# Kernel tuning notes

Hardware: AMD Instinct MI355X
Metric: run time of the kernel (lower is better)

## Reference

```python
import jax, jax.numpy as jnp
import numpy as np

D_MODEL = 1024
HEADS = 16
HEAD_DIM = D_MODEL // HEADS
D_FF = 4096
ADA_DIM = 16
GAMMA_SCALE = 1.0
LN_EPS = 1e-5
ROPE_BASE = 10000.0


def setup_inputs() -> dict:
    key = jax.random.key(0)
    ks = jax.random.split(key, 20)
    s = 0.02
    B, S = 4, 1024
    inp = {
        "src_reps": jax.random.normal(ks[0], (B, S, D_MODEL), jnp.float32),
        "src_mask": jnp.ones((B, S), dtype=bool),
        "compact_style": jax.random.normal(ks[1], (B, ADA_DIM), jnp.float32),
        # adaLN modulation params (stored as [in, out]; torch Linear uses [out, in])
        "ada0_w": jax.random.normal(ks[2], (ADA_DIM, 3 * D_MODEL), jnp.float32) * s,
        "ada0_b": jax.random.normal(ks[3], (3 * D_MODEL,), jnp.float32) * s,
        "ada1_w": jax.random.normal(ks[4], (ADA_DIM, 3 * D_MODEL), jnp.float32) * s,
        "ada1_b": jax.random.normal(ks[5], (3 * D_MODEL,), jnp.float32) * s,
        # attention params
        "wq": jax.random.normal(ks[6], (D_MODEL, D_MODEL), jnp.float32) * s,
        "bq": jnp.zeros((D_MODEL,), jnp.float32),
        "wk": jax.random.normal(ks[7], (D_MODEL, D_MODEL), jnp.float32) * s,
        "bk": jnp.zeros((D_MODEL,), jnp.float32),
        "wv": jax.random.normal(ks[8], (D_MODEL, D_MODEL), jnp.float32) * s,
        "bv": jnp.zeros((D_MODEL,), jnp.float32),
        "wo": jax.random.normal(ks[9], (D_MODEL, D_MODEL), jnp.float32) * s,
        "bo": jnp.zeros((D_MODEL,), jnp.float32),
        # FFN params
        "w1": jax.random.normal(ks[10], (D_MODEL, D_FF), jnp.float32) * s,
        "b1": jnp.zeros((D_FF,), jnp.float32),
        "w2": jax.random.normal(ks[11], (D_FF, D_MODEL), jnp.float32) * s,
        "b2": jnp.zeros((D_MODEL,), jnp.float32),
    }
    return inp


def _layernorm(x):
    mu = jnp.mean(x, axis=-1, keepdims=True)
    var = jnp.var(x, axis=-1, keepdims=True)
    return (x - mu) * jax.lax.rsqrt(var + LN_EPS)


def _rope(x):
    # x: (B, H, S, Dh). Llama rotary: rotate-half formulation.
    S, d = x.shape[-2], x.shape[-1]
    inv_freq = 1.0 / (ROPE_BASE ** (jnp.arange(0, d, 2, dtype=jnp.float32) / d))
    freqs = jnp.arange(S, dtype=jnp.float32)[:, None] * inv_freq[None, :]  # (S, d/2)
    emb = jnp.concatenate([freqs, freqs], axis=-1)  # (S, d)
    cos, sin = jnp.cos(emb), jnp.sin(emb)
    x1, x2 = x[..., : d // 2], x[..., d // 2:]
    rot = jnp.concatenate([-x2, x1], axis=-1)
    return x * cos + rot * sin


def _mha(x, mask, wq, bq, wk, bk, wv, bv, wo, bo):
    B, S, _ = x.shape
    def split_heads(t):
        return t.reshape(B, S, HEADS, HEAD_DIM).transpose(0, 2, 1, 3)  # (B,H,S,Dh)
    q = split_heads(x @ wq + bq)
    k = split_heads(x @ wk + bk)
    v = split_heads(x @ wv + bv)
    q = _rope(q)
    k = _rope(k)
    scores = jnp.einsum("bhqd,bhkd->bhqk", q, k) / np.sqrt(HEAD_DIM).astype(np.float32)
    scores = jnp.where(mask[:, None, None, :], scores, -jnp.inf)
    attn = jax.nn.softmax(scores, axis=-1)
    out = jnp.einsum("bhqk,bhkd->bhqd", attn, v)
    out = out.transpose(0, 2, 1, 3).reshape(B, S, D_MODEL)
    return out @ wo + bo


def _adaln(x, compact_style, ada_w, ada_b, sublayer):
    style = jax.nn.silu(compact_style) @ ada_w + ada_b  # (B, 3*D)
    gamma, beta, alpha = jnp.split(style, 3, axis=-1)
    gamma = jnp.tanh(gamma) * GAMMA_SCALE
    normed = (1.0 + gamma[:, None, :]) * _layernorm(x) + beta[:, None, :]
    return x + alpha[:, None, :] * sublayer(normed)


def reference(src_reps, src_mask, compact_style,
              ada0_w, ada0_b, ada1_w, ada1_b,
              wq, bq, wk, bk, wv, bv, wo, bo,
              w1, b1, w2, b2):
    attn_fn = lambda t: _mha(t, src_mask, wq, bq, wk, bk, wv, bv, wo, bo)
    ffn_fn = lambda t: jax.nn.gelu(t @ w1 + b1, approximate=False) @ w2 + b2
    x = _adaln(src_reps, compact_style, ada0_w, ada0_b, attn_fn)
    x = _adaln(x, compact_style, ada1_w, ada1_b, ffn_fn)
    return x
```

## Files before the change

### kernel.cpp

```cpp
#include <hip/hip_runtime.h>
#include <hip/hip_bf16.h>
#include <cstdint>
#include <cstddef>

typedef short short8 __attribute__((ext_vector_type(8)));
typedef float f32x4 __attribute__((ext_vector_type(4)));
typedef __hip_bfloat16 bf16;

static __device__ __forceinline__ void gload_lds16(const void* g, void* l) {
    __builtin_amdgcn_global_load_lds((__attribute__((address_space(1))) void*)(g),
                                     (__attribute__((address_space(3))) void*)(l),
                                     16, 0, 0);
}

__global__ void prep_kernel(const float* __restrict__ cs,
                            const float* __restrict__ a0w, const float* __restrict__ a0b,
                            const float* __restrict__ a1w, const float* __restrict__ a1b,
                            const float* __restrict__ bq, const float* __restrict__ bk,
                            const float* __restrict__ bv,
                            float* __restrict__ styles, float* __restrict__ bqkv,
                            float* __restrict__ ropec, float* __restrict__ ropes) {
    int idx = blockIdx.x * 256 + threadIdx.x;
    if (idx < 24576) {
        int L = idx / 12288;
        int rem = idx - L * 12288;
        int b = rem / 3072;
        int j = rem - b * 3072;
        const float* w = L ? a1w : a0w;
        const float* bb = L ? a1b : a0b;
        float acc = bb[j];
        #pragma unroll
        for (int i = 0; i < 16; ++i) {
            float c = cs[b * 16 + i];
            float s = c / (1.f + expf(-c));
            acc += s * w[i * 3072 + j];
        }
        if (j < 1024) acc = tanhf(acc);
        styles[L * 12288 + b * 3072 + j] = acc;
    } else if (idx < 27648) {
        int j = idx - 24576;
        bqkv[j] = (j < 1024) ? bq[j] : (j < 2048 ? bk[j - 1024] : bv[j - 2048]);
    } else if (idx < 27648 + 32768) {
        int t = idx - 27648;
        int s = t >> 5, j = t & 31;
        float f = (float)s * powf(10000.f, -(float)j / 32.f);
        ropec[t] = cosf(f);
        ropes[t] = sinf(f);
    }
}

__global__ __launch_bounds__(256) void transpose_all(const float* __restrict__ wq,
                                                     const float* __restrict__ wk,
                                                     const float* __restrict__ wv,
                                                     const float* __restrict__ wo,
                                                     const float* __restrict__ w1,
                                                     const float* __restrict__ w2,
                                                     bf16* __restrict__ WQKV,
                                                     bf16* __restrict__ WOT,
                                                     bf16* __restrict__ W1T,
                                                     bf16* __restrict__ W2T) {
    __shared__ float t[32][33];
    const int bid = blockIdx.x;
    const float* src; bf16* dst; int R, C, br, bc;
    if (bid < 1024)      { src = wq; dst = WQKV;                 R = 1024; C = 1024; br = bid >> 5;            bc = bid & 31; }
    else if (bid < 2048) { src = wk; dst = WQKV + 1024 * 1024;   R = 1024; C = 1024; br = (bid - 1024) >> 5;   bc = bid & 31; }
    else if (bid < 3072) { src = wv; dst = WQKV + 2048 * 1024;   R = 1024; C = 1024; br = (bid - 2048) >> 5;   bc = bid & 31; }
    else if (bid < 4096) { src = wo; dst = WOT;                  R = 1024; C = 1024; br = (bid - 3072) >> 5;   bc = bid & 31; }
    else if (bid < 8192) { int u = bid - 4096; src = w1; dst = W1T; R = 1024; C = 4096; br = u >> 7; bc = u & 127; }
    else                 { int u = bid - 8192; src = w2; dst = W2T; R = 4096; C = 1024; br = u >> 5; bc = u & 31; }
    const int tx = threadIdx.x & 31, ty = threadIdx.x >> 5;
    const int r0 = br * 32, c0 = bc * 32;
    #pragma unroll
    for (int i = 0; i < 4; ++i)
        t[ty + i * 8][tx] = src[(size_t)(r0 + ty + i * 8) * C + c0 + tx];
    __syncthreads();
    #pragma unroll
    for (int i = 0; i < 4; ++i)
        dst[(size_t)(c0 + ty + i * 8) * R + r0 + tx] = __float2bfloat16(t[tx][ty + i * 8]);
}

__global__ __launch_bounds__(256) void adaln_kernel(const float* __restrict__ x,
                                                    const float* __restrict__ style,
                                                    bf16* __restrict__ out) {
    const int row = blockIdx.x;
    const int b = row >> 10;
    const int tid = threadIdx.x;
    const float4 v = ((const float4*)(x + (size_t)row * 1024))[tid];
    float s = v.x + v.y + v.z + v.w;
    float ss = v.x * v.x + v.y * v.y + v.z * v.z + v.w * v.w;
    #pragma unroll
    for (int o = 32; o > 0; o >>= 1) { s += __shfl_down(s, o); ss += __shfl_down(ss, o); }
    __shared__ float red[8];
    const int wave = tid >> 6, lane = tid & 63;
    if (lane == 0) { red[wave] = s; red[4 + wave] = ss; }
    __syncthreads();
    s = red[0] + red[1] + red[2] + red[3];
    ss = red[4] + red[5] + red[6] + red[7];
    const float mu = s * (1.f / 1024.f);
    const float rstd = rsqrtf(ss * (1.f / 1024.f) - mu * mu + 1e-5f);
    const float* st = style + b * 3072;
    bf16 tmp[4];
    const float vals[4] = {v.x, v.y, v.z, v.w};
    #pragma unroll
    for (int j = 0; j < 4; ++j) {
        int d = tid * 4 + j;
        float g = st[d];
        float be = st[1024 + d];
        tmp[j] = __float2bfloat16((1.f + g) * ((vals[j] - mu) * rstd) + be);
    }
    *(ushort4*)(out + (size_t)row * 1024 + tid * 4) = *(ushort4*)tmp;
}

template <int MODE>
__global__ __launch_bounds__(256) void gemm_kernel(const bf16* __restrict__ A,
                                                   const bf16* __restrict__ Bt,
                                                   int M, int N, int K,
                                                   const float* __restrict__ bias,
                                                   bf16* __restrict__ o0,
                                                   bf16* __restrict__ o1,
                                                   bf16* __restrict__ o2,
                                                   const float* __restrict__ rc,
                                                   const float* __restrict__ rs) {
    __shared__ __align__(16) bf16 As[2][128 * 32];
    __shared__ __align__(16) bf16 Bs[2][128 * 32];
    const int tid = threadIdx.x;
    const int wave = tid >> 6, lane = tid & 63;
    const int lg = lane >> 4, lr = lane & 15;
    const int row0 = blockIdx.x * 128, col0 = blockIdx.y * 128;
    const int wr = (wave >> 1) * 64, wc = (wave & 1) * 64;

    f32x4 acc[4][4];
    #pragma unroll
    for (int i = 0; i < 4; ++i)
        #pragma unroll
        for (int j = 0; j < 4; ++j) acc[i][j] = f32x4{0.f, 0.f, 0.f, 0.f};

    const int sr = tid >> 2;
    const int sc = (tid & 3) * 8;

    #define STAGE_128(b_, kt_)                                                        \
        {                                                                             \
            _Pragma("unroll")                                                         \
            for (int is = 0; is < 2; ++is) {                                          \
                gload_lds16(A + (size_t)(row0 + is * 64 + sr) * K + (kt_) + sc,       \
                            (char*)As[b_] + (is * 256 + wave * 64) * 16);             \
                gload_lds16(Bt + (size_t)(col0 + is * 64 + sr) * K + (kt_) + sc,      \
                            (char*)Bs[b_] + (is * 256 + wave * 64) * 16);             \
            }                                                                         \
        }

    const int nt = K >> 5;
    STAGE_128(0, 0);
    for (int t = 0; t < nt; ++t) {
        const int cur = t & 1;
        if (t + 1 < nt) {
            STAGE_128(cur ^ 1, (t + 1) * 32);
            asm volatile("s_waitcnt vmcnt(4)" ::: "memory");
        } else {
            asm volatile("s_waitcnt vmcnt(0)" ::: "memory");
        }
        __builtin_amdgcn_s_barrier();
        short8 af[4], bfr[4];
        #pragma unroll
        for (int i = 0; i < 4; ++i) {
            af[i] = *(const short8*)(As[cur] + (wr + i * 16 + lr) * 32 + lg * 8);
            bfr[i] = *(const short8*)(Bs[cur] + (wc + i * 16 + lr) * 32 + lg * 8);
        }
        #pragma unroll
        for (int mi = 0; mi < 4; ++mi)
            #pragma unroll
            for (int ni = 0; ni < 4; ++ni)
                acc[mi][ni] = __builtin_amdgcn_mfma_f32_16x16x32_bf16(af[mi], bfr[ni],
                                                                      acc[mi][ni], 0, 0, 0);
        __builtin_amdgcn_s_barrier();
    }
    #undef STAGE_128

    if constexpr (MODE == 0) {
        const int colbase = col0 + wc;
        if (colbase < 2048) {
            bf16* dst = (colbase < 1024) ? o0 : o1;
            const int h = (colbase >> 6) & 15;
            #pragma unroll
            for (int mi = 0; mi < 4; ++mi) {
                #pragma unroll
                for (int n2 = 0; n2 < 2; ++n2) {
                    const int jj = n2 * 16 + lr;
                    const float bv1 = bias[colbase + jj];
                    const float bv2 = bias[colbase + 32 + jj];
                    #pragma unroll
                    for (int j = 0; j < 4; ++j) {
                        const int row = row0 + wr + mi * 16 + lg * 4 + j;
                        const int bb = row >> 10, ssi = row & 1023;
                        const float c = rc[ssi * 32 + jj];
                        const float sn = rs[ssi * 32 + jj];
                        const float x1 = acc[mi][n2][j] + bv1;
                        const float x2 = acc[mi][n2 + 2][j] + bv2;
                        bf16* base = dst + (((size_t)(bb * 16 + h) * 1024) + ssi) * 64;
                        base[jj] = __float2bfloat16(x1 * c - x2 * sn);
                        base[32 + jj] = __float2bfloat16(x2 * c + x1 * sn);
                    }
                }
            }
        } else {
            #pragma unroll
            for (int mi = 0; mi < 4; ++mi)
                #pragma unroll
                for (int ni = 0; ni < 4; ++ni)
                    #pragma unroll
                    for (int j = 0; j < 4; ++j) {
                        const int row = row0 + wr + mi * 16 + lg * 4 + j;
                        const int col = col0 + wc + ni * 16 + lr;
                        const float v = acc[mi][ni][j] + bias[col];
                        const int cv = col - 2048;
                        const int hh = cv >> 6, dd = cv & 63;
                        const int bb = row >> 10, ssi = row & 1023;
                        o2[(((size_t)bb * 16 + hh) * 64 + dd) * 1024 + ssi] = __float2bfloat16(v);
                    }
        }
    }
}

__global__ __launch_bounds__(512, 2) void gemm_ffn1(const bf16* __restrict__ A,
                                                    const bf16* __restrict__ Bt,
                                                    const float* __restrict__ bias,
                                                    bf16* __restrict__ o0) {
    __shared__ __align__(16) bf16 Abuf[4][256 * 32];
    __shared__ __align__(16) bf16 Bbuf[4][256 * 32];
    const int K = 1024;
    const int tid = threadIdx.x;
    const int lane = tid & 63;
    const int lg = lane >> 4, lr = lane & 15;
    const int wave = tid >> 6;
    const int wm = wave >> 2, wn = wave & 3;
    const int row0 = blockIdx.x * 256, col0 = blockIdx.y * 256;

    f32x4 acc[8][4];
    #pragma unroll
    for (int i = 0; i < 8; ++i)
        #pragma unroll
        for (int j = 0; j < 4; ++j) acc[i][j] = f32x4{0.f, 0.f, 0.f, 0.f};

    const int strow = tid >> 2;
    const int stpos = tid & 3;

    #define STG256(b_, kt_)                                                           \
        {                                                                             \
            _Pragma("unroll")                                                         \
            for (int it = 0; it < 2; ++it) {                                          \
                const int r_ = it * 128 + strow;                                      \
                const int sc_ = (kt_) + ((stpos ^ ((r_ >> 1) & 3)) * 8);              \
                gload_lds16(A + (size_t)(row0 + r_) * K + sc_,                        \
                            (char*)Abuf[b_] + (it * 512 + tid) * 16);                 \
                gload_lds16(Bt + (size_t)(col0 + r_) * K + sc_,                       \
                            (char*)Bbuf[b_] + (it * 512 + tid) * 16);                 \
            }                                                                         \
        }

    #define FFN_COMPUTE(cur_)                                                         \
        {                                                                             \
            short8 a_[8], b_[4];                                                      \
            _Pragma("unroll")                                                         \
            for (int i = 0; i < 8; ++i) {                                             \
                const int ra = wm * 128 + i * 16 + lr;                                \
                a_[i] = *(const short8*)((const char*)Abuf[cur_] + ra * 64 +          \
                                         ((lg ^ ((ra >> 1) & 3)) * 16));              \
            }                                                                         \
            _Pragma("unroll")                                                         \
            for (int j = 0; j < 4; ++j) {                                             \
                const int rb = wn * 64 + j * 16 + lr;                                 \
                b_[j] = *(const short8*)((const char*)Bbuf[cur_] + rb * 64 +          \
                                         ((lg ^ ((rb >> 1) & 3)) * 16));              \
            }                                                                         \
            __builtin_amdgcn_s_setprio(1);                                            \
            _Pragma("unroll")                                                         \
            for (int i = 0; i < 8; ++i)                                               \
                _Pragma("unroll")                                                     \
                for (int j = 0; j < 4; ++j)                                           \
                    acc[i][j] = __builtin_amdgcn_mfma_f32_16x16x32_bf16(              \
                        a_[i], b_[j], acc[i][j], 0, 0, 0);                            \
            __builtin_amdgcn_s_setprio(0);                                            \
        }

    STG256(0, 0);
    STG256(1, 32);
    STG256(2, 64);
    for (int u = 0; u < 7; ++u) {
        const int t0 = u * 4;
        STG256(3, (t0 + 3) * 32);
        asm volatile("s_waitcnt vmcnt(12)" ::: "memory");
        __builtin_amdgcn_s_barrier();
        FFN_COMPUTE(0);
        __builtin_amdgcn_s_barrier();
        STG256(0, (t0 + 4) * 32);
        asm volatile("s_waitcnt vmcnt(12)" ::: "memory");
        __builtin_amdgcn_s_barrier();
        FFN_COMPUTE(1);
        __builtin_amdgcn_s_barrier();
        STG256(1, (t0 + 5) * 32);
        asm volatile("s_waitcnt vmcnt(12)" ::: "memory");
        __builtin_amdgcn_s_barrier();
        FFN_COMPUTE(2);
        __builtin_amdgcn_s_barrier();
        STG256(2, (t0 + 6) * 32);
        asm volatile("s_waitcnt vmcnt(12)" ::: "memory");
        __builtin_amdgcn_s_barrier();
        FFN_COMPUTE(3);
        __builtin_amdgcn_s_barrier();
    }
    STG256(3, 31 * 32);
    asm volatile("s_waitcnt vmcnt(12)" ::: "memory");
    __builtin_amdgcn_s_barrier();
    FFN_COMPUTE(0);
    __builtin_amdgcn_s_barrier();
    asm volatile("s_waitcnt vmcnt(8)" ::: "memory");
    __builtin_amdgcn_s_barrier();
    FFN_COMPUTE(1);
    __builtin_amdgcn_s_barrier();
    asm volatile("s_waitcnt vmcnt(4)" ::: "memory");
    __builtin_amdgcn_s_barrier();
    FFN_COMPUTE(2);
    __builtin_amdgcn_s_barrier();
    asm volatile("s_waitcnt vmcnt(0)" ::: "memory");
    __builtin_amdgcn_s_barrier();
    FFN_COMPUTE(3);
    #undef STG256
    #undef FFN_COMPUTE

    #pragma unroll
    for (int i = 0; i < 8; ++i)
        #pragma unroll
        for (int j = 0; j < 4; ++j)
            #pragma unroll
            for (int jj = 0; jj < 4; ++jj) {
                const int row = row0 + wm * 128 + i * 16 + lg * 4 + jj;
                const int col = col0 + wn * 64 + j * 16 + lr;
                const float v = acc[i][j][jj] + bias[col];
                const float y = 1.5957692f * v * fmaf(0.044715f, v * v, 1.f);
                const float g = v / (1.f + exp2f(-1.44269504f * y));
                o0[(size_t)row * 4096 + col] = __float2bfloat16(g);
            }
}

template <int RES>
__global__ __launch_bounds__(256) void gemm_skinny(const bf16* __restrict__ A,
                                                   const bf16* __restrict__ Bt,
                                                   int K,
                                                   const float* __restrict__ bias,
                                                   const float* __restrict__ style,
                                                   const float* __restrict__ resid,
                                                   float* __restrict__ out_f) {
    __shared__ __align__(16) bf16 As[2][64 * 64];
    __shared__ __align__(16) bf16 Bs[2][64 * 64];
    const int tid = threadIdx.x;
    const int wave = tid >> 6, lane = tid & 63;
    const int lg = lane >> 4, lr = lane & 15;
    const int row0 = blockIdx.x * 64, col0 = blockIdx.y * 64;
    const int wr2 = (wave >> 1) * 32, wc2 = (wave & 1) * 32;

    f32x4 acc[2][2];
    #pragma unroll
    for (int i = 0; i < 2; ++i)
        #pragma unroll
        for (int j = 0; j < 2; ++j) acc[i][j] = f32x4{0.f, 0.f, 0.f, 0.f};

    const int strow = tid >> 3;
    const int stslot = tid & 7;

    #define STAGE_64(b_, kt_)                                                         \
        {                                                                             \
            _Pragma("unroll")                                                         \
            for (int it = 0; it < 2; ++it) {                                          \
                const int r_ = strow + it * 32;                                       \
                const int scol_ = (kt_) + ((stslot ^ (r_ & 7)) * 8);                  \
                gload_lds16(A + (size_t)(row0 + r_) * K + scol_,                      \
                            (char*)As[b_] + it * 4096 + tid * 16);                    \
                gload_lds16(Bt + (size_t)(col0 + r_) * K + scol_,                     \
                            (char*)Bs[b_] + it * 4096 + tid * 16);                    \
            }                                                                         \
        }

    const int nt = K >> 6;
    STAGE_64(0, 0);
    for (int t = 0; t < nt; ++t) {
        const int cur = t & 1;
        if (t + 1 < nt) {
            STAGE_64(cur ^ 1, (t + 1) * 64);
            asm volatile("s_waitcnt vmcnt(4)" ::: "memory");
        } else {
            asm volatile("s_waitcnt vmcnt(0)" ::: "memory");
        }
        __builtin_amdgcn_s_barrier();
        #pragma unroll
        for (int kk2 = 0; kk2 < 2; ++kk2) {
            short8 a[2], b[2];
            #pragma unroll
            for (int i = 0; i < 2; ++i) {
                const int ra = wr2 + i * 16 + lr;
                const int rb = wc2 + i * 16 + lr;
                a[i] = *(const short8*)((const char*)As[cur] + ra * 128 +
                                        (((kk2 * 4 + lg) ^ (ra & 7)) * 16));
                b[i] = *(const short8*)((const char*)Bs[cur] + rb * 128 +
                                        (((kk2 * 4 + lg) ^ (rb & 7)) * 16));
            }
            #pragma unroll
            for (int mi = 0; mi < 2; ++mi)
                #pragma unroll
                for (int ni = 0; ni < 2; ++ni)
                    acc[mi][ni] = __builtin_amdgcn_mfma_f32_16x16x32_bf16(a[mi], b[ni],
                                                                          acc[mi][ni], 0, 0, 0);
        }
        __builtin_amdgcn_s_barrier();
    }
    #undef STAGE_64

    #pragma unroll
    for (int mi = 0; mi < 2; ++mi)
        #pragma unroll
        for (int ni = 0; ni < 2; ++ni)
            #pragma unroll
            for (int j = 0; j < 4; ++j) {
                const int row = row0 + wr2 + mi * 16 + lg * 4 + j;
                const int col = col0 + wc2 + ni * 16 + lr;
                const int bb = row >> 10;
                const float a = style[bb * 3072 + 2048 + col];
                const float v = acc[mi][ni][j] + bias[col];
                if constexpr (RES == 0)
                    out_f[(size_t)row * 1024 + col] = resid[(size_t)row * 1024 + col] + a * v;
                else
                    out_f[(size_t)row * 1024 + col] += a * v;
            }
}

#define SWZ3(r_) ((((r_) & 7) + 2 * (((r_) >> 3) & 7)) & 7)

__global__ __launch_bounds__(512) void attn_kernel(const bf16* __restrict__ qtb,
                                                   const bf16* __restrict__ ktb,
                                                   const bf16* __restrict__ vtb,
                                                   bf16* __restrict__ obuf) {
    __shared__ __align__(16) bf16 Klds[2][64 * 64];
    __shared__ __align__(16) bf16 Vlds[2][64 * 64];
    const int bh = blockIdx.x;
    const int tid = threadIdx.x;
    const int wave = tid >> 6, lane = tid & 63;
    const int lg = lane >> 4, lr = lane & 15;
    const int q0 = blockIdx.y * 128 + wave * 16;

    const bf16* qbase = qtb + ((size_t)bh * 1024 + q0) * 64;
    const bf16* kg = ktb + (size_t)bh * 1024 * 64;
    const bf16* vg = vtb + (size_t)bh * 64 * 1024;

    const short8 qa0 = *(const short8*)(qbase + (size_t)lr * 64 + lg * 8);
    const short8 qa1 = *(const short8*)(qbase + (size_t)lr * 64 + 32 + lg * 8);

    f32x4 of[4];
    #pragma unroll
    for (int df = 0; df < 4; ++df) of[df] = f32x4{0.f, 0.f, 0.f, 0.f};
    float lsum = 0.f;

    const float Cs = 0.125f * 1.44269504f;
    const float SH = 28.853900817f;
    const int kp = 8 * (lr >> 2) + (lr & 3);

    const int strow = tid >> 3;
    const int stslot = tid & 7;
    const int stcs = (stslot + 8 - SWZ3(strow)) & 7;

    #define ATT_STAGE(b_, kt_)                                                       \
        {                                                                            \
            gload_lds16(kg + (size_t)((kt_) + strow) * 64 + stcs * 8,                \
                        (char*)Klds[b_] + tid * 16);                                 \
            gload_lds16(vg + (size_t)strow * 1024 + (kt_) + stcs * 8,                \
                        (char*)Vlds[b_] + tid * 16);                                 \
        }

    #define LDK(b_, r_, cs_)                                                         \
        (*(const short8*)(Klds[b_] + (r_) * 64 + ((((cs_) + SWZ3(r_)) & 7) * 8)))
    #define LDV(b_, r_, cs_)                                                         \
        (*(const short8*)(Vlds[b_] + (r_) * 64 + ((((cs_) + SWZ3(r_)) & 7) * 8)))

    #define ATT_STEP(b_, ktl_)                                                       \
        {                                                                            \
            const int r0_ = (ktl_) + kp, r1_ = r0_ + 4;                              \
            const short8 k00_ = LDK(b_, r0_, lg);                                    \
            const short8 k01_ = LDK(b_, r0_, 4 + lg);                                \
            const short8 k10_ = LDK(b_, r1_, lg);                                    \
            const short8 k11_ = LDK(b_, r1_, 4 + lg);                                \
            const int vcs_ = ((ktl_) >> 3) + lg;                                     \
            const short8 v0_ = LDV(b_, lr, vcs_);                                    \
            const short8 v1_ = LDV(b_, 16 + lr, vcs_);                               \
            const short8 v2_ = LDV(b_, 32 + lr, vcs_);                               \
            const short8 v3_ = LDV(b_, 48 + lr, vcs_);                               \
            f32x4 s0_ = __builtin_amdgcn_mfma_f32_16x16x32_bf16(                     \
                k00_, qa0, f32x4{0.f, 0.f, 0.f, 0.f}, 0, 0, 0);                      \
            s0_ = __builtin_amdgcn_mfma_f32_16x16x32_bf16(k01_, qa1, s0_, 0, 0, 0);  \
            f32x4 s1_ = __builtin_amdgcn_mfma_f32_16x16x32_bf16(                     \
                k10_, qa0, f32x4{0.f, 0.f, 0.f, 0.f}, 0, 0, 0);                      \
            s1_ = __builtin_amdgcn_mfma_f32_16x16x32_bf16(k11_, qa1, s1_, 0, 0, 0);  \
            ushort us_[8];                                                           \
            _Pragma("unroll")                                                        \
            for (int j_ = 0; j_ < 4; ++j_) {                                         \
                const float p0_ = exp2f(fmaf(s0_[j_], Cs, -SH));                     \
                const float p1_ = exp2f(fmaf(s1_[j_], Cs, -SH));                     \
                lsum += p0_ + p1_;                                                   \
                us_[j_] = __bfloat16_as_ushort(__float2bfloat16(p0_));               \
                us_[4 + j_] = __bfloat16_as_ushort(__float2bfloat16(p1_));           \
            }                                                                        \
            short8 pa_;                                                              \
            _Pragma("unroll")                                                        \
            for (int j_ = 0; j_ < 8; ++j_) pa_[j_] = (short)us_[j_];                 \
            of[0] = __builtin_amdgcn_mfma_f32_16x16x32_bf16(pa_, v0_, of[0], 0, 0, 0); \
            of[1] = __builtin_amdgcn_mfma_f32_16x16x32_bf16(pa_, v1_, of[1], 0, 0, 0); \
            of[2] = __builtin_amdgcn_mfma_f32_16x16x32_bf16(pa_, v2_, of[2], 0, 0, 0); \
            of[3] = __builtin_amdgcn_mfma_f32_16x16x32_bf16(pa_, v3_, of[3], 0, 0, 0); \
        }

    ATT_STAGE(0, 0);
    for (int t = 0; t < 16; ++t) {
        const int cur = t & 1;
        if (t < 15) {
            ATT_STAGE(cur ^ 1, (t + 1) * 64);
            asm volatile("s_waitcnt vmcnt(2)" ::: "memory");
        } else {
            asm volatile("s_waitcnt vmcnt(0)" ::: "memory");
        }
        __builtin_amdgcn_s_barrier();
        ATT_STEP(cur, 0);
        ATT_STEP(cur, 32);
        __builtin_amdgcn_s_barrier();
    }
    #undef ATT_STAGE
    #undef ATT_STEP
    #undef LDK
    #undef LDV

    float tsum = lsum;
    tsum += __shfl_xor(tsum, 16);
    tsum += __shfl_xor(tsum, 32);
    float rcpv[4];
    #pragma unroll
    for (int j = 0; j < 4; ++j)
        rcpv[j] = 1.f / __shfl(tsum, lg * 4 + j);

    const int b = bh >> 4, h = bh & 15;
    #pragma unroll
    for (int df = 0; df < 4; ++df)
        #pragma unroll
        for (int j = 0; j < 4; ++j) {
            const int q = q0 + lg * 4 + j;
            obuf[((size_t)b * 1024 + q) * 1024 + h * 64 + df * 16 + lr] =
                __float2bfloat16(of[df][j] * rcpv[j]);
        }
}

extern "C" void kernel_launch(void* const* d_in, const int* in_sizes, int n_in,
                              void* d_out, int out_size, void* d_ws, size_t ws_size,
                              hipStream_t stream) {
    const float* src = (const float*)d_in[0];
    const float* cs  = (const float*)d_in[2];
    const float* a0w = (const float*)d_in[3];
    const float* a0b = (const float*)d_in[4];
    const float* a1w = (const float*)d_in[5];
    const float* a1b = (const float*)d_in[6];
    const float* wq  = (const float*)d_in[7];
    const float* bq  = (const float*)d_in[8];
    const float* wk  = (const float*)d_in[9];
    const float* bk  = (const float*)d_in[10];
    const float* wv  = (const float*)d_in[11];
    const float* bv  = (const float*)d_in[12];
    const float* wo  = (const float*)d_in[13];
    const float* bo  = (const float*)d_in[14];
    const float* w1  = (const float*)d_in[15];
    const float* b1  = (const float*)d_in[16];
    const float* w2  = (const float*)d_in[17];
    const float* b2  = (const float*)d_in[18];
    float* out = (float*)d_out;

    if (ws_size < 67481600u) return;

    char* ws = (char*)d_ws;
    bf16*  WQKV = (bf16*)(ws + 0);
    bf16*  WOT  = (bf16*)(ws + 6291456);
    bf16*  W1T  = (bf16*)(ws + 8388608);
    bf16*  W2T  = (bf16*)(ws + 16777216);
    float* STY  = (float*)(ws + 25165824);
    float* BQKV = (float*)(ws + 25264128);
    float* RC   = (float*)(ws + 25276416);
    float* RS   = (float*)(ws + 25407488);
    bf16*  NORM = (bf16*)(ws + 25538560);
    bf16*  QT   = (bf16*)(ws + 33927168);
    bf16*  KT   = (bf16*)(ws + 42315776);
    bf16*  VT   = (bf16*)(ws + 50704384);
    bf16*  OBUF = (bf16*)(ws + 59092992);
    bf16*  HID  = (bf16*)(ws + 33927168);

    prep_kernel<<<237, 256, 0, stream>>>(cs, a0w, a0b, a1w, a1b, bq, bk, bv, STY, BQKV, RC, RS);
    transpose_all<<<12288, 256, 0, stream>>>(wq, wk, wv, wo, w1, w2, WQKV, WOT, W1T, W2T);

    adaln_kernel<<<4096, 256, 0, stream>>>(src, STY, NORM);
    gemm_kernel<0><<<dim3(32, 24), 256, 0, stream>>>(NORM, WQKV, 4096, 3072, 1024, BQKV,
                                                     QT, KT, VT, RC, RS);
    attn_kernel<<<dim3(64, 8), 512, 0, stream>>>(QT, KT, VT, OBUF);
    gemm_skinny<0><<<dim3(64, 16), 256, 0, stream>>>(OBUF, WOT, 1024, bo, STY, src, out);
    adaln_kernel<<<4096, 256, 0, stream>>>(out, STY + 12288, NORM);
    gemm_ffn1<<<dim3(16, 16), 512, 0, stream>>>(NORM, W1T, b1, HID);
    gemm_skinny<1><<<dim3(64, 16), 256, 0, stream>>>(HID, W2T, 4096, b2, STY + 12288, nullptr, out);
}
```

Measured before the change: 226.1 us.

## Deepen A-tile prefetch in skinny GEMM to triple-buffered staggered pipeline

The skinny GEMM used for the output projection and the FFN down-projection now triple-buffers the A tile and issues A loads two k-tiles ahead while B stays double-buffered one tile ahead. The main loop is unrolled by six so that buffer indices are compile-time constants. This is meant to hide more global-load latency behind the MFMA work. It uses more LDS and relies on nt-4 being divisible by 6, which holds for K=1024 (nt=16) and K=4096 (nt=64); other K values would break.

```diff
diff --git a/kernel.cpp b/kernel.cpp
--- a/kernel.cpp
+++ b/kernel.cpp
@@ -350,7 +350,7 @@
                                                    const float* __restrict__ style,
                                                    const float* __restrict__ resid,
                                                    float* __restrict__ out_f) {
-    __shared__ __align__(16) bf16 As[2][64 * 64];
+    __shared__ __align__(16) bf16 As[3][64 * 64];
     __shared__ __align__(16) bf16 Bs[2][64 * 64];
     const int tid = threadIdx.x;
     const int wave = tid >> 6, lane = tid & 63;
@@ -367,7 +367,7 @@
     const int strow = tid >> 3;
     const int stslot = tid & 7;
 
-    #define STAGE_64(b_, kt_)                                                         \
+    #define STA64(b_, kt_)                                                            \
         {                                                                             \
             _Pragma("unroll")                                                         \
             for (int it = 0; it < 2; ++it) {                                          \
@@ -375,44 +375,82 @@
                 const int scol_ = (kt_) + ((stslot ^ (r_ & 7)) * 8);                  \
                 gload_lds16(A + (size_t)(row0 + r_) * K + scol_,                      \
                             (char*)As[b_] + it * 4096 + tid * 16);                    \
+            }                                                                         \
+        }
+    #define STB64(b_, kt_)                                                            \
+        {                                                                             \
+            _Pragma("unroll")                                                         \
+            for (int it = 0; it < 2; ++it) {                                          \
+                const int r_ = strow + it * 32;                                       \
+                const int scol_ = (kt_) + ((stslot ^ (r_ & 7)) * 8);                  \
                 gload_lds16(Bt + (size_t)(col0 + r_) * K + scol_,                     \
                             (char*)Bs[b_] + it * 4096 + tid * 16);                    \
             }                                                                         \
         }
 
+    #define SKCOMP(ab_, bb_)                                                          \
+        {                                                                             \
+            _Pragma("unroll")                                                         \
+            for (int kk2 = 0; kk2 < 2; ++kk2) {                                       \
+                short8 a_[2], b_[2];                                                  \
+                _Pragma("unroll")                                                     \
+                for (int i = 0; i < 2; ++i) {                                         \
+                    const int ra = wr2 + i * 16 + lr;                                 \
+                    const int rb = wc2 + i * 16 + lr;                                 \
+                    a_[i] = *(const short8*)((const char*)As[ab_] + ra * 128 +        \
+                                             (((kk2 * 4 + lg) ^ (ra & 7)) * 16));     \
+                    b_[i] = *(const short8*)((const char*)Bs[bb_] + rb * 128 +        \
+                                             (((kk2 * 4 + lg) ^ (rb & 7)) * 16));     \
+                }                                                                     \
+                _Pragma("unroll")                                                     \
+                for (int mi = 0; mi < 2; ++mi)                                        \
+                    _Pragma("unroll")                                                 \
+                    for (int ni = 0; ni < 2; ++ni)                                    \
+                        acc[mi][ni] = __builtin_amdgcn_mfma_f32_16x16x32_bf16(        \
+                            a_[mi], b_[ni], acc[mi][ni], 0, 0, 0);                    \
+            }                                                                         \
+        }
+
+    #define SKSTEP(Bn_, kb_, An_, ka_, Ac_, Bc_, vm_)                                 \
+        {                                                                             \
+            STB64(Bn_, (kb_) * 64);                                                   \
+            STA64(An_, (ka_) * 64);                                                   \
+            asm volatile("s_waitcnt vmcnt(" #vm_ ")" ::: "memory");                   \
+            __builtin_amdgcn_s_barrier();                                             \
+            SKCOMP(Ac_, Bc_);                                                         \
+            __builtin_amdgcn_s_barrier();                                             \
+        }
+
     const int nt = K >> 6;
-    STAGE_64(0, 0);
-    for (int t = 0; t < nt; ++t) {
-        const int cur = t & 1;
-        if (t + 1 < nt) {
-            STAGE_64(cur ^ 1, (t + 1) * 64);
-            asm volatile("s_waitcnt vmcnt(4)" ::: "memory");
-        } else {
-            asm volatile("s_waitcnt vmcnt(0)" ::: "memory");
-        }
-        __builtin_amdgcn_s_barrier();
-        #pragma unroll
-        for (int kk2 = 0; kk2 < 2; ++kk2) {
-            short8 a[2], b[2];
-            #pragma unroll
-            for (int i = 0; i < 2; ++i) {
-                const int ra = wr2 + i * 16 + lr;
-                const int rb = wc2 + i * 16 + lr;
-                a[i] = *(const short8*)((const char*)As[cur] + ra * 128 +
-                                        (((kk2 * 4 + lg) ^ (ra & 7)) * 16));
-                b[i] = *(const short8*)((const char*)Bs[cur] + rb * 128 +
-                                        (((kk2 * 4 + lg) ^ (rb & 7)) * 16));
-            }
-            #pragma unroll
-            for (int mi = 0; mi < 2; ++mi)
-                #pragma unroll
-                for (int ni = 0; ni < 2; ++ni)
-                    acc[mi][ni] = __builtin_amdgcn_mfma_f32_16x16x32_bf16(a[mi], b[ni],
-                                                                          acc[mi][ni], 0, 0, 0);
-        }
-        __builtin_amdgcn_s_barrier();
-    }
-    #undef STAGE_64
+    STA64(0, 0);
+    STB64(0, 0);
+    STA64(1, 64);
+    for (int u = 0; u < (nt - 4) / 6; ++u) {
+        const int t0 = u * 6;
+        SKSTEP(1, t0 + 1, 2, t0 + 2, 0, 0, 6);
+        SKSTEP(0, t0 + 2, 0, t0 + 3, 1, 1, 6);
+        SKSTEP(1, t0 + 3, 1, t0 + 4, 2, 0, 6);
+        SKSTEP(0, t0 + 4, 2, t0 + 5, 0, 1, 6);
+        SKSTEP(1, t0 + 5, 0, t0 + 6, 1, 0, 6);
+        SKSTEP(0, t0 + 6, 1, t0 + 7, 2, 1, 6);
+    }
+    {
+        const int tb = nt - 4;
+        SKSTEP(1, tb + 1, 2, tb + 2, 0, 0, 6);
+        SKSTEP(0, tb + 2, 0, tb + 3, 1, 1, 6);
+        STB64(1, (tb + 3) * 64);
+        asm volatile("s_waitcnt vmcnt(4)" ::: "memory");
+        __builtin_amdgcn_s_barrier();
+        SKCOMP(2, 0);
+        __builtin_amdgcn_s_barrier();
+        asm volatile("s_waitcnt vmcnt(0)" ::: "memory");
+        __builtin_amdgcn_s_barrier();
+        SKCOMP(0, 1);
+    }
+    #undef SKSTEP
+    #undef SKCOMP
+    #undef STA64
+    #undef STB64
 
     #pragma unroll
     for (int mi = 0; mi < 2; ++mi)
```

New measurement: 223.7 us. About the same (-1.1%).
